# Optimization experiments

Measured on AMD Instinct MI355X. Metric: run time of the kernel, lower is better.

Reference implementation:

```python
import jax, jax.numpy as jnp
import numpy as np

D = 192          # d_model
H = 8            # n_heads
DH = D // H      # d_head = 24
DFF = 2 * D      # FeedForward hidden = d_model*2
SIZES = [384 + 8 * i for i in range(32)]   # ragged segment lengths
TOTAL = sum(SIZES)                          # 16256
EPS = 1e-5

# static ragged -> padded index maps (numpy, baked at trace time)
_sz = np.asarray(SIZES)
B = len(_sz)
MAXN = int(_sz.max())
SEG = np.repeat(np.arange(B), _sz)                      # [TOTAL] segment id
POS = np.concatenate([np.arange(s) for s in _sz])       # [TOTAL] position in segment
PADMASK = np.ones((B, MAXN), dtype=bool)                # True = padding (key_padding_mask)
PADMASK[SEG, POS] = False


def _layernorm(x, gamma, beta):
    mu = jnp.mean(x, axis=-1, keepdims=True)
    var = jnp.var(x, axis=-1, keepdims=True)
    return (x - mu) * jax.lax.rsqrt(var + EPS) * gamma + beta


def setup_inputs() -> dict:
    key = jax.random.key(0)
    ks = jax.random.split(key, 8)
    w = lambda k, shape: jax.random.normal(k, shape, jnp.float32) * 0.02
    return {
        "x": jax.random.normal(ks[0], (TOTAL, D), jnp.float32),
        "sizes": jnp.asarray(SIZES, jnp.int32),
        "Wqkv": w(ks[1], (3 * D, D)), "bqkv": jnp.zeros((3 * D,), jnp.float32),
        "Wo": w(ks[2], (D, D)),       "bo": jnp.zeros((D,), jnp.float32),
        "Wg": w(ks[3], (D, 2 * D)),   "bg": jnp.zeros((D,), jnp.float32),
        "gamma1": jnp.ones((D,), jnp.float32), "beta1": jnp.zeros((D,), jnp.float32),
        "W1": w(ks[4], (DFF, D)),     "b1": jnp.zeros((DFF,), jnp.float32),
        "W2": w(ks[5], (D, DFF)),     "b2": jnp.zeros((D,), jnp.float32),
        "gamma2": jnp.ones((D,), jnp.float32), "beta2": jnp.zeros((D,), jnp.float32),
    }


def reference(x, sizes, Wqkv, bqkv, Wo, bo, Wg, bg, gamma1, beta1,
              W1, b1, W2, b2, gamma2, beta2):
    # --- pad_by_sizes (vectorized scatter, static index maps) ---
    pad = jnp.zeros((B, MAXN, D), x.dtype).at[SEG, POS].set(x)   # [B, MAXN, D]

    # --- nn.MultiheadAttention (batch_first, key_padding_mask) ---
    qkv = pad @ Wqkv.T + bqkv                                    # [B, MAXN, 3D]
    q, k, v = jnp.split(qkv, 3, axis=-1)
    def heads(t):  # [B, MAXN, D] -> [B, H, MAXN, DH]
        return t.reshape(B, MAXN, H, DH).transpose(0, 2, 1, 3)
    q, k, v = heads(q), heads(k), heads(v)
    scores = jnp.einsum("bhqd,bhkd->bhqk", q, k) / np.sqrt(DH)   # [B, H, MAXN, MAXN]
    scores = jnp.where(PADMASK[:, None, None, :], jnp.float32(-1e9), scores)
    attn = jax.nn.softmax(scores, axis=-1)
    o = jnp.einsum("bhqk,bhkd->bhqd", attn, v)                   # [B, H, MAXN, DH]
    o = o.transpose(0, 2, 1, 3).reshape(B, MAXN, D)
    out = o @ Wo.T + bo                                          # [B, MAXN, D]

    # --- gather back to ragged; gate/norm/ff are per-token, so the torch
    # per-segment loop is equivalent to one vectorized pass over all tokens ---
    out_flat = out[SEG, POS]                                     # [TOTAL, D]
    g = jax.nn.sigmoid(jnp.concatenate([out_flat, x], axis=-1) @ Wg.T + bg)
    h = g * out_flat + (1.0 - g) * x                             # GatedResidual
    h = _layernorm(h, gamma1, beta1)                             # self.norm
    y = jax.nn.silu(h @ W1.T + b1) @ W2.T + b2                   # FeedForward.net
    return _layernorm(h + y, gamma2, beta2)                      # residual + norm
```

## Files before the change

### kernel.cpp

```cpp
#include <hip/hip_runtime.h>
#include <math.h>

#define D_      192
#define H_      8
#define DH_     24
#define NSEG    32
#define TOTAL_  16256
static constexpr float LN_EPS = 1e-5f;
static constexpr float SCALE  = 0.20412414523193154f;
static constexpr float SC_L2E = 0.29446679331797463f;

typedef float  f32x4  __attribute__((ext_vector_type(4)));
typedef short  bf16x8 __attribute__((ext_vector_type(8)));
typedef unsigned short u16x4 __attribute__((ext_vector_type(4)));

__device__ __forceinline__ unsigned short f2b(float f) {
    union { float f; unsigned u; } v; v.f = f;
    unsigned r = v.u + 0x7FFFu + ((v.u >> 16) & 1u);
    return (unsigned short)(r >> 16);
}
__device__ __forceinline__ unsigned short f2b_fast(float f) {
    union { float f; unsigned u; } v; v.f = f;
    return (unsigned short)((v.u + 0x8000u) >> 16);
}
__device__ __forceinline__ float b2f(unsigned short h) {
    union { unsigned u; float f; } v; v.u = (unsigned)h << 16; return v.f;
}
__device__ __forceinline__ float fexp2(float x) {
#if __has_builtin(__builtin_amdgcn_exp2f)
    return __builtin_amdgcn_exp2f(x);
#else
    return exp2f(x);
#endif
}

#define NXE 3121152
__global__ __launch_bounds__(256)
void conv_all(const float* __restrict__ x,
              const float* __restrict__ w0, const float* __restrict__ w1,
              const float* __restrict__ w2, const float* __restrict__ w3,
              const float* __restrict__ w4,
              unsigned short* __restrict__ xb, unsigned short* __restrict__ wb)
{
    int i = (blockIdx.x * 256 + threadIdx.x) * 4;
    const float* src; unsigned short* dst; int off;
    if (i < NXE) { src = x; dst = xb; off = 0; }
    else {
        int j = i - NXE; dst = wb;
        if      (j < 110592) { src = w0; off = 0; }
        else if (j < 147456) { src = w1; off = 110592; }
        else if (j < 221184) { src = w2; off = 147456; }
        else if (j < 294912) { src = w3; off = 221184; }
        else                 { src = w4; off = 294912; }
        i = j;
    }
    float4 v = *(const float4*)&src[i - off];
    u16x4 o = { f2b(v.x), f2b(v.y), f2b(v.z), f2b(v.w) };
    *(u16x4*)&dst[i] = o;
}

template<int KF, int MR, int EPI, int OUT_BF16>
__global__ __launch_bounds__(256)
void gemm_lds(const unsigned short* __restrict__ A0,
              const unsigned short* __restrict__ Wb,
              const float* __restrict__ bias,
              void* __restrict__ Cout, int N)
{
    constexpr int KSW = KF * 32 + 8;
    __shared__ unsigned short Wp[64 * KSW];

    const int tid = threadIdx.x;
    const int wv  = tid >> 6;
    const int l   = tid & 63;
    const int m0  = blockIdx.x * (64 * MR) + wv * (16 * MR);
    const int n0  = blockIdx.y * 64;
    const int rl  = l & 15;
    const int kc  = (l >> 4) * 8;

    bf16x8 afrag[MR][KF];
    #pragma unroll
    for (int h = 0; h < MR; ++h)
        #pragma unroll
        for (int kk = 0; kk < KF; ++kk)
            afrag[h][kk] = *(const bf16x8*)&A0[(size_t)(m0 + h * 16 + rl) * (KF * 32) + kk * 32 + kc];

    #pragma unroll
    for (int i = 0; i < KF; ++i) {
        int u = i * 256 + tid;
        int row = u / (KF * 4), c = u % (KF * 4);
        bf16x8 wv8 = *(const bf16x8*)&Wb[(size_t)(n0 + row) * (KF * 32) + c * 8];
        *(bf16x8*)&Wp[row * KSW + c * 8] = wv8;
    }
    __syncthreads();

    f32x4 acc[MR][4] = {};
    #pragma unroll
    for (int kk = 0; kk < KF; ++kk) {
        #pragma unroll
        for (int nf = 0; nf < 4; ++nf) {
            bf16x8 b = *(const bf16x8*)&Wp[(nf * 16 + rl) * KSW + kk * 32 + kc];
            #pragma unroll
            for (int h = 0; h < MR; ++h)
                acc[h][nf] = __builtin_amdgcn_mfma_f32_16x16x32_bf16(afrag[h][kk], b, acc[h][nf], 0, 0, 0);
        }
    }

    #pragma unroll
    for (int h = 0; h < MR; ++h) {
        #pragma unroll
        for (int nf = 0; nf < 4; ++nf) {
            const int c = n0 + nf * 16 + rl;
            const float bz = bias[c];
            #pragma unroll
            for (int q = 0; q < 4; ++q) {
                const int r = m0 + h * 16 + (l >> 4) * 4 + q;
                float v = acc[h][nf][q] + bz;
                if (EPI == 1) { float s = 1.f / (1.f + __expf(-v)); v = v * s; }
                if (OUT_BF16) ((unsigned short*)Cout)[(size_t)r * N + c] = f2b(v);
                else          ((float*)Cout)[(size_t)r * N + c] = v;
            }
        }
    }
}

template<int KF, int DUAL, int EPI>
__global__ __launch_bounds__(256)
void gemm_ln(const unsigned short* __restrict__ A0,
             const unsigned short* __restrict__ A1,
             const unsigned short* __restrict__ Wb,
             const float* __restrict__ bias,
             const unsigned short* __restrict__ e0b,
             const float* __restrict__ e1,
             const float* __restrict__ gamma, const float* __restrict__ beta,
             float* __restrict__ outf, unsigned short* __restrict__ outb)
{
    constexpr int KSW = 72;
    __shared__ unsigned short Wp[192 * KSW];

    const int tid = threadIdx.x;
    const int wv  = tid >> 6;
    const int l   = tid & 63;
    const int m0  = blockIdx.x * 64 + wv * 16;
    const int rl  = l & 15;
    const int kc  = (l >> 4) * 8;

    bf16x8 afrag[KF];
    #pragma unroll
    for (int kk = 0; kk < KF; ++kk) {
        int k = kk * 32 + kc;
        const unsigned short* ap;
        if (DUAL) {
            const int half = KF * 16;
            ap = (k < half) ? &A0[(size_t)(m0 + rl) * half + k]
                            : &A1[(size_t)(m0 + rl) * half + (k - half)];
        } else {
            ap = &A0[(size_t)(m0 + rl) * (KF * 32) + k];
        }
        afrag[kk] = *(const bf16x8*)ap;
    }

    f32x4 acc[12] = {};
    #pragma unroll
    for (int ks = 0; ks < KF / 2; ++ks) {
        __syncthreads();
        #pragma unroll
        for (int i = 0; i < 6; ++i) {
            int u = i * 256 + tid;
            int row = u >> 3, c = u & 7;
            bf16x8 wv8 = *(const bf16x8*)&Wb[(size_t)row * (KF * 32) + ks * 64 + c * 8];
            *(bf16x8*)&Wp[row * KSW + c * 8] = wv8;
        }
        __syncthreads();
        #pragma unroll
        for (int k2 = 0; k2 < 2; ++k2) {
            #pragma unroll
            for (int nf = 0; nf < 12; ++nf) {
                bf16x8 b = *(const bf16x8*)&Wp[(nf * 16 + rl) * KSW + k2 * 32 + kc];
                acc[nf] = __builtin_amdgcn_mfma_f32_16x16x32_bf16(afrag[ks * 2 + k2], b, acc[nf], 0, 0, 0);
            }
        }
    }

    float bz[12], gam[12], bet[12];
    #pragma unroll
    for (int nf = 0; nf < 12; ++nf) {
        bz[nf]  = bias[nf * 16 + rl];
        gam[nf] = gamma[nf * 16 + rl];
        bet[nf] = beta[nf * 16 + rl];
    }

    #pragma unroll
    for (int q = 0; q < 4; ++q) {
        const int r = m0 + (l >> 4) * 4 + q;
        const size_t rb = (size_t)r * 192;
        float h[12];
        float s = 0.f;
        #pragma unroll
        for (int nf = 0; nf < 12; ++nf) {
            const int c = nf * 16 + rl;
            float v = acc[nf][q] + bz[nf];
            if (EPI == 2) {
                float g = 1.f / (1.f + __expf(-v));
                h[nf] = g * b2f(e0b[rb + c]) + (1.f - g) * e1[rb + c];
            } else {
                h[nf] = v + e1[rb + c];
            }
            s += h[nf];
        }
        s += __shfl_xor(s, 1); s += __shfl_xor(s, 2);
        s += __shfl_xor(s, 4); s += __shfl_xor(s, 8);
        const float mu = s * (1.f / 192.f);
        float sq = 0.f;
        #pragma unroll
        for (int nf = 0; nf < 12; ++nf) { float d = h[nf] - mu; sq += d * d; }
        sq += __shfl_xor(sq, 1); sq += __shfl_xor(sq, 2);
        sq += __shfl_xor(sq, 4); sq += __shfl_xor(sq, 8);
        const float rstd = rsqrtf(sq * (1.f / 192.f) + LN_EPS);
        #pragma unroll
        for (int nf = 0; nf < 12; ++nf) {
            const int c = nf * 16 + rl;
            float rv = (h[nf] - mu) * rstd * gam[nf] + bet[nf];
            outf[rb + c] = rv;
            if (EPI == 2) outb[rb + c] = f2b(rv);
        }
    }
}

#define KSTR 40
#define VSTR 72
#define PSTR 72

__global__ __launch_bounds__(256)
void attn_mfma(const unsigned short* __restrict__ qkv, unsigned short* __restrict__ o)
{
    const int seg  = blockIdx.z;
    const int head = blockIdx.y;
    const int n    = 384 + 8 * seg;
    const int base = 384 * seg + 4 * seg * (seg - 1);
    const int q0   = blockIdx.x * 128;
    if (q0 >= n) return;

    __shared__ unsigned short Ks[64 * KSTR];
    __shared__ unsigned short Vt[32 * VSTR];
    __shared__ unsigned short Pl[4][32 * PSTR];

    const int tid = threadIdx.x;
    const int wv  = tid >> 6;
    const int l   = tid & 63;
    const int lq  = l & 15;
    const int g   = l >> 4;

    if (tid < 64) *(uint4*)&Ks[tid * KSTR + 24] = make_uint4(0, 0, 0, 0);
    for (int t4 = tid; t4 < 144; t4 += 256)
        *(unsigned long long*)&Vt[24 * VSTR + t4 * 4] = 0ull;

    int   qrow[2];
    bf16x8 qfrag[2];
    #pragma unroll
    for (int qf = 0; qf < 2; ++qf) {
        qrow[qf] = q0 + wv * 32 + qf * 16 + lq;
        const int qtok = base + (qrow[qf] < n ? qrow[qf] : n - 1);
        bf16x8 qz = {};
        if (g < 3) qz = *(const bf16x8*)&qkv[(size_t)qtok * 576 + head * 24 + g * 8];
        qfrag[qf] = qz;
    }

    float lsum[2] = {0.f, 0.f};
    f32x4 oacc[2][2] = {};

    const int nt = (n + 63) >> 6;
    for (int t = 0; t < nt; ++t) {
        const int j0 = t * 64;
        __syncthreads();
        if (tid < 192) {
            const int j = tid & 63;
            const int c = tid >> 6;
            int jr = j0 + j; if (jr >= n) jr = n - 1;
            const unsigned short* rp = &qkv[(size_t)(base + jr) * 576 + head * 24 + c * 8];
            bf16x8 kv = *(const bf16x8*)(rp + 192);
            *(bf16x8*)&Ks[j * KSTR + c * 8] = kv;
            bf16x8 vv = *(const bf16x8*)(rp + 384);
            #pragma unroll
            for (int e = 0; e < 8; ++e)
                Vt[(c * 8 + e) * VSTR + j] = ((const unsigned short*)&vv)[e];
        }
        __syncthreads();

        const int rem = n - j0;
        #pragma unroll
        for (int qf = 0; qf < 2; ++qf) {
            f32x4 sacc[4] = {};
            #pragma unroll
            for (int ks = 0; ks < 4; ++ks) {
                bf16x8 kf = *(const bf16x8*)&Ks[(ks * 16 + lq) * KSTR + g * 8];
                sacc[ks] = __builtin_amdgcn_mfma_f32_16x16x32_bf16(kf, qfrag[qf], sacc[ks], 0, 0, 0);
            }
            float psum = 0.f;
            unsigned short pb[16];
            #pragma unroll
            for (int ks = 0; ks < 4; ++ks) {
                #pragma unroll
                for (int r = 0; r < 4; ++r) {
                    float p = fexp2(sacc[ks][r] * SC_L2E);
                    if (rem < 64) { int key = ks * 16 + g * 4 + r; if (key >= rem) p = 0.f; }
                    psum += p;
                    pb[ks * 4 + r] = f2b_fast(p);
                }
            }
            psum += __shfl_xor(psum, 16);
            psum += __shfl_xor(psum, 32);
            lsum[qf] += psum;
            #pragma unroll
            for (int ks = 0; ks < 4; ++ks) {
                u16x4 w4 = { pb[ks*4+0], pb[ks*4+1], pb[ks*4+2], pb[ks*4+3] };
                *(u16x4*)&Pl[wv][(qf * 16 + lq) * PSTR + ks * 16 + g * 4] = w4;
            }
        }
        asm volatile("s_waitcnt lgkmcnt(0)" ::: "memory");
        __builtin_amdgcn_sched_barrier(0);

        #pragma unroll
        for (int jk = 0; jk < 2; ++jk) {
            bf16x8 vf[2];
            #pragma unroll
            for (int df = 0; df < 2; ++df)
                vf[df] = *(const bf16x8*)&Vt[(df * 16 + lq) * VSTR + jk * 32 + g * 8];
            #pragma unroll
            for (int qf = 0; qf < 2; ++qf) {
                bf16x8 pf = *(const bf16x8*)&Pl[wv][(qf * 16 + lq) * PSTR + jk * 32 + g * 8];
                #pragma unroll
                for (int df = 0; df < 2; ++df)
                    oacc[qf][df] = __builtin_amdgcn_mfma_f32_16x16x32_bf16(vf[df], pf, oacc[qf][df], 0, 0, 0);
            }
        }
    }

    #pragma unroll
    for (int qf = 0; qf < 2; ++qf) {
        if (qrow[qf] < n) {
            const float rl2 = 1.f / lsum[qf];
            #pragma unroll
            for (int df = 0; df < 2; ++df) {
                const int d0 = df * 16 + g * 4;
                if (d0 < 24) {
                    u16x4 r = { f2b_fast(oacc[qf][df][0] * rl2), f2b_fast(oacc[qf][df][1] * rl2),
                                f2b_fast(oacc[qf][df][2] * rl2), f2b_fast(oacc[qf][df][3] * rl2) };
                    *(u16x4*)&o[(size_t)(base + qrow[qf]) * 192 + head * 24 + d0] = r;
                }
            }
        }
    }
}

extern "C" void kernel_launch(void* const* d_in, const int* in_sizes, int n_in,
                              void* d_out, int out_size, void* d_ws, size_t ws_size,
                              hipStream_t stream)
{
    const float* x      = (const float*)d_in[0];
    const float* Wqkv   = (const float*)d_in[2];
    const float* bqkv   = (const float*)d_in[3];
    const float* Wo     = (const float*)d_in[4];
    const float* bo     = (const float*)d_in[5];
    const float* Wg     = (const float*)d_in[6];
    const float* bg     = (const float*)d_in[7];
    const float* gamma1 = (const float*)d_in[8];
    const float* beta1  = (const float*)d_in[9];
    const float* W1     = (const float*)d_in[10];
    const float* b1     = (const float*)d_in[11];
    const float* W2     = (const float*)d_in[12];
    const float* b2     = (const float*)d_in[13];
    const float* gamma2 = (const float*)d_in[14];
    const float* beta2  = (const float*)d_in[15];
    float* out = (float*)d_out;
    float* ws  = (float*)d_ws;

    const size_t T = TOTAL_;
    unsigned short* qkv_b = (unsigned short*)ws;
    unsigned short* ff1_b = (unsigned short*)ws;
    unsigned short* o_b   = (unsigned short*)(ws + 288 * T);
    unsigned short* att_b = (unsigned short*)(ws + 384 * T);
    unsigned short* xb    = (unsigned short*)(ws + 480 * T);
    unsigned short* wb    = (unsigned short*)(ws + 576 * T);
    float*          h1    = ws + 588 * T;
    unsigned short* h1b   = (unsigned short*)(ws + 780 * T);

    dim3 blk(256);

    conv_all<<<dim3(3408), blk, 0, stream>>>(x, Wqkv, Wo, Wg, W1, W2, xb, wb);
    gemm_lds<6,2,0,1><<<dim3(127, 9), blk, 0, stream>>>(xb, wb, bqkv, qkv_b, 576);
    attn_mfma<<<dim3(5, H_, NSEG), blk, 0, stream>>>(qkv_b, o_b);
    gemm_lds<6,2,0,1><<<dim3(127, 3), blk, 0, stream>>>(o_b, wb + 110592, bo, att_b, 192);
    gemm_ln<12,1,2><<<dim3(254), blk, 0, stream>>>(att_b, xb, wb + 147456, bg,
                                                   att_b, x, gamma1, beta1, h1, h1b);
    gemm_lds<6,2,1,1><<<dim3(127, 6), blk, 0, stream>>>(h1b, wb + 221184, b1, ff1_b, 384);
    gemm_ln<12,0,3><<<dim3(254), blk, 0, stream>>>(ff1_b, nullptr, wb + 294912, b2,
                                                   nullptr, h1, gamma2, beta2, out, nullptr);
}
```

Measured before the change: 108.8 us.

## Fuse Wo+gate+LN1 and FFN+LN2 into single kernels; convert x on the fly

The Wo projection is fused with the gated residual GEMM and LayerNorm1 into one kernel that keeps the attention output in LDS. Both FFN GEMMs plus LayerNorm2 are fused the same way, with the SiLU intermediate held in LDS. The QKV GEMM now reads fp32 x directly and packs it to bf16 in registers, which removes the separate bf16 copy of x. This cuts launches and global round-trips for the att, ff1 and xb buffers. In exchange, each block uses more LDS with 254 blocks at one block per CU, which lowers occupancy and can leave CUs idle.

```diff
diff --git a/kernel.cpp b/kernel.cpp
--- a/kernel.cpp
+++ b/kernel.cpp
@@ -33,35 +33,37 @@
     return exp2f(x);
 #endif
 }
-
-#define NXE 3121152
+__device__ __forceinline__ bf16x8 ldpack8(const float* p) {
+    float4 a0 = *(const float4*)p;
+    float4 a1 = *(const float4*)(p + 4);
+    bf16x8 r;
+    ((unsigned short*)&r)[0] = f2b(a0.x); ((unsigned short*)&r)[1] = f2b(a0.y);
+    ((unsigned short*)&r)[2] = f2b(a0.z); ((unsigned short*)&r)[3] = f2b(a0.w);
+    ((unsigned short*)&r)[4] = f2b(a1.x); ((unsigned short*)&r)[5] = f2b(a1.y);
+    ((unsigned short*)&r)[6] = f2b(a1.z); ((unsigned short*)&r)[7] = f2b(a1.w);
+    return r;
+}
+
 __global__ __launch_bounds__(256)
-void conv_all(const float* __restrict__ x,
-              const float* __restrict__ w0, const float* __restrict__ w1,
-              const float* __restrict__ w2, const float* __restrict__ w3,
-              const float* __restrict__ w4,
-              unsigned short* __restrict__ xb, unsigned short* __restrict__ wb)
+void conv_w(const float* __restrict__ w0, const float* __restrict__ w1,
+            const float* __restrict__ w2, const float* __restrict__ w3,
+            const float* __restrict__ w4, unsigned short* __restrict__ out)
 {
     int i = (blockIdx.x * 256 + threadIdx.x) * 4;
-    const float* src; unsigned short* dst; int off;
-    if (i < NXE) { src = x; dst = xb; off = 0; }
-    else {
-        int j = i - NXE; dst = wb;
-        if      (j < 110592) { src = w0; off = 0; }
-        else if (j < 147456) { src = w1; off = 110592; }
-        else if (j < 221184) { src = w2; off = 147456; }
-        else if (j < 294912) { src = w3; off = 221184; }
-        else                 { src = w4; off = 294912; }
-        i = j;
-    }
+    const float* src; int off;
+    if      (i < 110592) { src = w0; off = 0; }
+    else if (i < 147456) { src = w1; off = 110592; }
+    else if (i < 221184) { src = w2; off = 147456; }
+    else if (i < 294912) { src = w3; off = 221184; }
+    else                 { src = w4; off = 294912; }
     float4 v = *(const float4*)&src[i - off];
     u16x4 o = { f2b(v.x), f2b(v.y), f2b(v.z), f2b(v.w) };
-    *(u16x4*)&dst[i] = o;
-}
-
-template<int KF, int MR, int EPI, int OUT_BF16>
+    *(u16x4*)&out[i] = o;
+}
+
+template<int KF, int MR, int OUT_BF16, int AF32>
 __global__ __launch_bounds__(256)
-void gemm_lds(const unsigned short* __restrict__ A0,
+void gemm_lds(const void* __restrict__ Ain,
               const unsigned short* __restrict__ Wb,
               const float* __restrict__ bias,
               void* __restrict__ Cout, int N)
@@ -81,15 +83,18 @@
     #pragma unroll
     for (int h = 0; h < MR; ++h)
         #pragma unroll
-        for (int kk = 0; kk < KF; ++kk)
-            afrag[h][kk] = *(const bf16x8*)&A0[(size_t)(m0 + h * 16 + rl) * (KF * 32) + kk * 32 + kc];
+        for (int kk = 0; kk < KF; ++kk) {
+            if (AF32)
+                afrag[h][kk] = ldpack8((const float*)Ain + (size_t)(m0 + h * 16 + rl) * (KF * 32) + kk * 32 + kc);
+            else
+                afrag[h][kk] = *(const bf16x8*)((const unsigned short*)Ain + (size_t)(m0 + h * 16 + rl) * (KF * 32) + kk * 32 + kc);
+        }
 
     #pragma unroll
     for (int i = 0; i < KF; ++i) {
         int u = i * 256 + tid;
         int row = u / (KF * 4), c = u % (KF * 4);
-        bf16x8 wv8 = *(const bf16x8*)&Wb[(size_t)(n0 + row) * (KF * 32) + c * 8];
-        *(bf16x8*)&Wp[row * KSW + c * 8] = wv8;
+        *(bf16x8*)&Wp[row * KSW + c * 8] = *(const bf16x8*)&Wb[(size_t)(n0 + row) * (KF * 32) + c * 8];
     }
     __syncthreads();
 
@@ -115,7 +120,6 @@
             for (int q = 0; q < 4; ++q) {
                 const int r = m0 + h * 16 + (l >> 4) * 4 + q;
                 float v = acc[h][nf][q] + bz;
-                if (EPI == 1) { float s = 1.f / (1.f + __expf(-v)); v = v * s; }
                 if (OUT_BF16) ((unsigned short*)Cout)[(size_t)r * N + c] = f2b(v);
                 else          ((float*)Cout)[(size_t)r * N + c] = v;
             }
@@ -123,88 +127,121 @@
     }
 }
 
-template<int KF, int DUAL, int EPI>
-__global__ __launch_bounds__(256)
-void gemm_ln(const unsigned short* __restrict__ A0,
-             const unsigned short* __restrict__ A1,
-             const unsigned short* __restrict__ Wb,
-             const float* __restrict__ bias,
-             const unsigned short* __restrict__ e0b,
-             const float* __restrict__ e1,
-             const float* __restrict__ gamma, const float* __restrict__ beta,
-             float* __restrict__ outf, unsigned short* __restrict__ outb)
+__global__ __launch_bounds__(256, 1)
+void wo_gate_ln1(const unsigned short* __restrict__ o_b,
+                 const float* __restrict__ x,
+                 const unsigned short* __restrict__ wo_b,
+                 const unsigned short* __restrict__ wg_b,
+                 const float* __restrict__ bo, const float* __restrict__ bg,
+                 const float* __restrict__ gamma1, const float* __restrict__ beta1,
+                 float* __restrict__ h1, unsigned short* __restrict__ h1b)
 {
-    constexpr int KSW = 72;
-    __shared__ unsigned short Wp[192 * KSW];
+    constexpr int WS = 200;
+    constexpr int AS = 200;
+    __shared__ unsigned short Wp[192 * WS];
+    __shared__ unsigned short Al[64 * AS];
 
     const int tid = threadIdx.x;
     const int wv  = tid >> 6;
     const int l   = tid & 63;
-    const int m0  = blockIdx.x * 64 + wv * 16;
     const int rl  = l & 15;
-    const int kc  = (l >> 4) * 8;
-
-    bf16x8 afrag[KF];
-    #pragma unroll
-    for (int kk = 0; kk < KF; ++kk) {
-        int k = kk * 32 + kc;
-        const unsigned short* ap;
-        if (DUAL) {
-            const int half = KF * 16;
-            ap = (k < half) ? &A0[(size_t)(m0 + rl) * half + k]
-                            : &A1[(size_t)(m0 + rl) * half + (k - half)];
-        } else {
-            ap = &A0[(size_t)(m0 + rl) * (KF * 32) + k];
-        }
-        afrag[kk] = *(const bf16x8*)ap;
-    }
-
-    f32x4 acc[12] = {};
-    #pragma unroll
-    for (int ks = 0; ks < KF / 2; ++ks) {
-        __syncthreads();
-        #pragma unroll
-        for (int i = 0; i < 6; ++i) {
-            int u = i * 256 + tid;
-            int row = u >> 3, c = u & 7;
-            bf16x8 wv8 = *(const bf16x8*)&Wb[(size_t)row * (KF * 32) + ks * 64 + c * 8];
-            *(bf16x8*)&Wp[row * KSW + c * 8] = wv8;
-        }
-        __syncthreads();
-        #pragma unroll
-        for (int k2 = 0; k2 < 2; ++k2) {
-            #pragma unroll
-            for (int nf = 0; nf < 12; ++nf) {
-                bf16x8 b = *(const bf16x8*)&Wp[(nf * 16 + rl) * KSW + k2 * 32 + kc];
-                acc[nf] = __builtin_amdgcn_mfma_f32_16x16x32_bf16(afrag[ks * 2 + k2], b, acc[nf], 0, 0, 0);
-            }
+    const int g   = l >> 4;
+    const int kc  = g * 8;
+    const int blk0 = blockIdx.x * 64;
+    const int m0   = blk0 + wv * 16;
+
+    bf16x8 afA[6];
+    #pragma unroll
+    for (int kk = 0; kk < 6; ++kk)
+        afA[kk] = *(const bf16x8*)&o_b[(size_t)(m0 + rl) * 192 + kk * 32 + kc];
+
+    #pragma unroll
+    for (int i = 0; i < 18; ++i) {
+        int u = i * 256 + tid;
+        int row = u / 24, c = u % 24;
+        *(bf16x8*)&Wp[row * WS + c * 8] = *(const bf16x8*)&wo_b[(size_t)row * 192 + c * 8];
+    }
+    __syncthreads();
+
+    f32x4 accA[12] = {};
+    #pragma unroll
+    for (int kk = 0; kk < 6; ++kk)
+        #pragma unroll
+        for (int nf = 0; nf < 12; ++nf) {
+            bf16x8 b = *(const bf16x8*)&Wp[(nf * 16 + rl) * WS + kk * 32 + kc];
+            accA[nf] = __builtin_amdgcn_mfma_f32_16x16x32_bf16(afA[kk], b, accA[nf], 0, 0, 0);
+        }
+
+    float att[12][4];
+    #pragma unroll
+    for (int nf = 0; nf < 12; ++nf) {
+        const float bz = bo[nf * 16 + rl];
+        #pragma unroll
+        for (int q = 0; q < 4; ++q) {
+            att[nf][q] = accA[nf][q] + bz;
+            const int row = wv * 16 + g * 4 + q;
+            Al[row * AS + nf * 16 + rl] = f2b(att[nf][q]);
+        }
+    }
+    __syncthreads();
+
+    #pragma unroll
+    for (int i = 0; i < 18; ++i) {
+        int u = i * 256 + tid;
+        int row = u / 24, c = u % 24;
+        *(bf16x8*)&Wp[row * WS + c * 8] = *(const bf16x8*)&wg_b[(size_t)row * 384 + c * 8];
+    }
+    __syncthreads();
+
+    f32x4 accB[12] = {};
+    #pragma unroll
+    for (int kk = 0; kk < 6; ++kk) {
+        bf16x8 a = *(const bf16x8*)&Al[(wv * 16 + rl) * AS + kk * 32 + kc];
+        #pragma unroll
+        for (int nf = 0; nf < 12; ++nf) {
+            bf16x8 b = *(const bf16x8*)&Wp[(nf * 16 + rl) * WS + kk * 32 + kc];
+            accB[nf] = __builtin_amdgcn_mfma_f32_16x16x32_bf16(a, b, accB[nf], 0, 0, 0);
+        }
+    }
+    __syncthreads();
+
+    #pragma unroll
+    for (int i = 0; i < 18; ++i) {
+        int u = i * 256 + tid;
+        int row = u / 24, c = u % 24;
+        *(bf16x8*)&Wp[row * WS + c * 8] = *(const bf16x8*)&wg_b[(size_t)row * 384 + 192 + c * 8];
+    }
+    __syncthreads();
+
+    #pragma unroll
+    for (int kk = 0; kk < 6; ++kk) {
+        bf16x8 a = ldpack8(&x[(size_t)(m0 + rl) * 192 + kk * 32 + kc]);
+        #pragma unroll
+        for (int nf = 0; nf < 12; ++nf) {
+            bf16x8 b = *(const bf16x8*)&Wp[(nf * 16 + rl) * WS + kk * 32 + kc];
+            accB[nf] = __builtin_amdgcn_mfma_f32_16x16x32_bf16(a, b, accB[nf], 0, 0, 0);
         }
     }
 
     float bz[12], gam[12], bet[12];
     #pragma unroll
     for (int nf = 0; nf < 12; ++nf) {
-        bz[nf]  = bias[nf * 16 + rl];
-        gam[nf] = gamma[nf * 16 + rl];
-        bet[nf] = beta[nf * 16 + rl];
-    }
-
+        bz[nf]  = bg[nf * 16 + rl];
+        gam[nf] = gamma1[nf * 16 + rl];
+        bet[nf] = beta1[nf * 16 + rl];
+    }
     #pragma unroll
     for (int q = 0; q < 4; ++q) {
-        const int r = m0 + (l >> 4) * 4 + q;
+        const int r = m0 + g * 4 + q;
         const size_t rb = (size_t)r * 192;
         float h[12];
         float s = 0.f;
         #pragma unroll
         for (int nf = 0; nf < 12; ++nf) {
             const int c = nf * 16 + rl;
-            float v = acc[nf][q] + bz[nf];
-            if (EPI == 2) {
-                float g = 1.f / (1.f + __expf(-v));
-                h[nf] = g * b2f(e0b[rb + c]) + (1.f - g) * e1[rb + c];
-            } else {
-                h[nf] = v + e1[rb + c];
-            }
+            float v  = accB[nf][q] + bz[nf];
+            float gt = 1.f / (1.f + __expf(-v));
+            h[nf] = gt * att[nf][q] + (1.f - gt) * x[rb + c];
             s += h[nf];
         }
         s += __shfl_xor(s, 1); s += __shfl_xor(s, 2);
@@ -220,8 +257,129 @@
         for (int nf = 0; nf < 12; ++nf) {
             const int c = nf * 16 + rl;
             float rv = (h[nf] - mu) * rstd * gam[nf] + bet[nf];
-            outf[rb + c] = rv;
-            if (EPI == 2) outb[rb + c] = f2b(rv);
+            h1[rb + c]  = rv;
+            h1b[rb + c] = f2b(rv);
+        }
+    }
+}
+
+__global__ __launch_bounds__(256, 1)
+void ffn_ln2(const unsigned short* __restrict__ h1b,
+             const float* __restrict__ h1,
+             const unsigned short* __restrict__ w1_b,
+             const unsigned short* __restrict__ w2_b,
+             const float* __restrict__ b1, const float* __restrict__ b2,
+             const float* __restrict__ gamma2, const float* __restrict__ beta2,
+             float* __restrict__ out)
+{
+    constexpr int WS = 200;
+    constexpr int FS = 392;
+    __shared__ unsigned short Wp[192 * WS];
+    __shared__ unsigned short Fl[64 * FS];
+
+    const int tid = threadIdx.x;
+    const int wv  = tid >> 6;
+    const int l   = tid & 63;
+    const int rl  = l & 15;
+    const int g   = l >> 4;
+    const int kc  = g * 8;
+    const int blk0 = blockIdx.x * 64;
+    const int m0   = blk0 + wv * 16;
+
+    bf16x8 afC[6];
+    #pragma unroll
+    for (int kk = 0; kk < 6; ++kk)
+        afC[kk] = *(const bf16x8*)&h1b[(size_t)(m0 + rl) * 192 + kk * 32 + kc];
+
+    f32x4 accC[24] = {};
+    #pragma unroll
+    for (int ch = 0; ch < 2; ++ch) {
+        if (ch) __syncthreads();
+        #pragma unroll
+        for (int i = 0; i < 18; ++i) {
+            int u = i * 256 + tid;
+            int row = u / 24, c = u % 24;
+            *(bf16x8*)&Wp[row * WS + c * 8] = *(const bf16x8*)&w1_b[(size_t)(ch * 192 + row) * 192 + c * 8];
+        }
+        __syncthreads();
+        #pragma unroll
+        for (int kk = 0; kk < 6; ++kk)
+            #pragma unroll
+            for (int nf = 0; nf < 12; ++nf) {
+                bf16x8 b = *(const bf16x8*)&Wp[(nf * 16 + rl) * WS + kk * 32 + kc];
+                accC[ch * 12 + nf] = __builtin_amdgcn_mfma_f32_16x16x32_bf16(afC[kk], b, accC[ch * 12 + nf], 0, 0, 0);
+            }
+    }
+    #pragma unroll
+    for (int ch = 0; ch < 2; ++ch)
+        #pragma unroll
+        for (int nf = 0; nf < 12; ++nf) {
+            const int col = ch * 192 + nf * 16 + rl;
+            const float bz = b1[col];
+            #pragma unroll
+            for (int q = 0; q < 4; ++q) {
+                float v = accC[ch * 12 + nf][q] + bz;
+                float s = 1.f / (1.f + __expf(-v));
+                const int row = wv * 16 + g * 4 + q;
+                Fl[row * FS + col] = f2b(v * s);
+            }
+        }
+    __syncthreads();
+
+    f32x4 accD[12] = {};
+    #pragma unroll
+    for (int ch = 0; ch < 2; ++ch) {
+        if (ch) __syncthreads();
+        #pragma unroll
+        for (int i = 0; i < 18; ++i) {
+            int u = i * 256 + tid;
+            int row = u / 24, c = u % 24;
+            *(bf16x8*)&Wp[row * WS + c * 8] = *(const bf16x8*)&w2_b[(size_t)row * 384 + ch * 192 + c * 8];
+        }
+        __syncthreads();
+        #pragma unroll
+        for (int kk = 0; kk < 6; ++kk) {
+            bf16x8 a = *(const bf16x8*)&Fl[(wv * 16 + rl) * FS + ch * 192 + kk * 32 + kc];
+            #pragma unroll
+            for (int nf = 0; nf < 12; ++nf) {
+                bf16x8 b = *(const bf16x8*)&Wp[(nf * 16 + rl) * WS + kk * 32 + kc];
+                accD[nf] = __builtin_amdgcn_mfma_f32_16x16x32_bf16(a, b, accD[nf], 0, 0, 0);
+            }
+        }
+    }
+
+    float bz[12], gam[12], bet[12];
+    #pragma unroll
+    for (int nf = 0; nf < 12; ++nf) {
+        bz[nf]  = b2[nf * 16 + rl];
+        gam[nf] = gamma2[nf * 16 + rl];
+        bet[nf] = beta2[nf * 16 + rl];
+    }
+    #pragma unroll
+    for (int q = 0; q < 4; ++q) {
+        const int r = m0 + g * 4 + q;
+        const size_t rb = (size_t)r * 192;
+        float h[12];
+        float s = 0.f;
+        #pragma unroll
+        for (int nf = 0; nf < 12; ++nf) {
+            const int c = nf * 16 + rl;
+            h[nf] = h1[rb + c] + accD[nf][q] + bz[nf];
+            s += h[nf];
+        }
+        s += __shfl_xor(s, 1); s += __shfl_xor(s, 2);
+        s += __shfl_xor(s, 4); s += __shfl_xor(s, 8);
+        const float mu = s * (1.f / 192.f);
+        float sq = 0.f;
+        #pragma unroll
+        for (int nf = 0; nf < 12; ++nf) { float d = h[nf] - mu; sq += d * d; }
+        sq += __shfl_xor(sq, 1); sq += __shfl_xor(sq, 2);
+        sq += __shfl_xor(sq, 4); sq += __shfl_xor(sq, 8);
+        const float rstd = rsqrtf(sq * (1.f / 192.f) + LN_EPS);
+        #pragma unroll
+        for (int nf = 0; nf < 12; ++nf) {
+            const int c = nf * 16 + rl;
+            out[rb + c] = (h[nf] - mu) * rstd * gam[nf] + bet[nf];
         }
     }
 }
@@ -376,23 +534,18 @@
 
     const size_t T = TOTAL_;
     unsigned short* qkv_b = (unsigned short*)ws;
-    unsigned short* ff1_b = (unsigned short*)ws;
     unsigned short* o_b   = (unsigned short*)(ws + 288 * T);
-    unsigned short* att_b = (unsigned short*)(ws + 384 * T);
-    unsigned short* xb    = (unsigned short*)(ws + 480 * T);
-    unsigned short* wb    = (unsigned short*)(ws + 576 * T);
-    float*          h1    = ws + 588 * T;
-    unsigned short* h1b   = (unsigned short*)(ws + 780 * T);
+    float*          h1    = ws + 384 * T;
+    unsigned short* h1b   = (unsigned short*)(ws + 576 * T);
+    unsigned short* wb    = (unsigned short*)(ws + 672 * T);
 
     dim3 blk(256);
 
-    conv_all<<<dim3(3408), blk, 0, stream>>>(x, Wqkv, Wo, Wg, W1, W2, xb, wb);
-    gemm_lds<6,2,0,1><<<dim3(127, 9), blk, 0, stream>>>(xb, wb, bqkv, qkv_b, 576);
+    conv_w<<<dim3(360), blk, 0, stream>>>(Wqkv, Wo, Wg, W1, W2, wb);
+    gemm_lds<6,2,1,1><<<dim3(127, 9), blk, 0, stream>>>(x, wb, bqkv, qkv_b, 576);
     attn_mfma<<<dim3(5, H_, NSEG), blk, 0, stream>>>(qkv_b, o_b);
-    gemm_lds<6,2,0,1><<<dim3(127, 3), blk, 0, stream>>>(o_b, wb + 110592, bo, att_b, 192);
-    gemm_ln<12,1,2><<<dim3(254), blk, 0, stream>>>(att_b, xb, wb + 147456, bg,
-                                                   att_b, x, gamma1, beta1, h1, h1b);
-    gemm_lds<6,2,1,1><<<dim3(127, 6), blk, 0, stream>>>(h1b, wb + 221184, b1, ff1_b, 384);
-    gemm_ln<12,0,3><<<dim3(254), blk, 0, stream>>>(ff1_b, nullptr, wb + 294912, b2,
-                                                   nullptr, h1, gamma2, beta2, out, nullptr);
-}
+    wo_gate_ln1<<<dim3(254), blk, 0, stream>>>(o_b, x, wb + 110592, wb + 147456,
+                                               bo, bg, gamma1, beta1, h1, h1b);
+    ffn_ln2<<<dim3(254), blk, 0, stream>>>(h1b, h1, wb + 221184, wb + 294912,
+                                           b1, b2, gamma2, beta2, out);
+}
```

New measurement: 105.1 us. 3.4% less time.
